# Kernel optimization log

Measured on AMD Instinct MI355X. Metric: run time of the kernel, lower is better.

The kernel has to match this reference:

```python
import jax, jax.numpy as jnp
import numpy as np

N = 50000      # nodes
E = 800000     # edges (avg degree 16)
IN, EMB, HID, OUT = 128, 256, 256, 128
KS = (25000, 12500)  # absolute top-k node counts per pooling level
NEG = -1e9


def setup_inputs() -> dict:
    key = jax.random.key(0)
    k = jax.random.split(key, 20)
    s = 0.05
    rn = lambda kk, shp: (jax.random.normal(kk, shp, jnp.float32) * s)
    return {
        "features": jax.random.normal(k[0], (N, IN), jnp.float32),
        "src": jax.random.randint(k[1], (E,), 0, N, dtype=jnp.int32),
        "dst": jax.random.randint(k[2], (E,), 0, N, dtype=jnp.int32),
        "W_embed": rn(k[3], (IN, EMB)), "b_embed": jnp.zeros((EMB,), jnp.float32),
        "W_enc0": rn(k[4], (EMB, HID)), "b_enc0": jnp.zeros((HID,), jnp.float32),
        "W_enc1": rn(k[5], (HID, HID)), "b_enc1": jnp.zeros((HID,), jnp.float32),
        "W_p0": rn(k[6], (HID, 1)), "b_p0": jnp.zeros((1,), jnp.float32),
        "W_p1": rn(k[7], (HID, 1)), "b_p1": jnp.zeros((1,), jnp.float32),
        "W_bot": rn(k[8], (HID, HID)), "b_bot": jnp.zeros((HID,), jnp.float32),
        "W_dec0": rn(k[9], (HID, HID)), "b_dec0": jnp.zeros((HID,), jnp.float32),
        "W_dec1": rn(k[10], (HID, OUT)), "b_dec1": jnp.zeros((OUT,), jnp.float32),
    }


def _gcn(h, src, dst, emask, W, b, act):
    """DGL GraphConv, norm='both': D_out^{-1/2} A D_in^{-1/2} h W + b, deg clamped >=1.
    emask: float [E] validity mask for edges of the current (sub)graph."""
    n = h.shape[0]
    deg_out = jnp.clip(jax.ops.segment_sum(emask, src, num_segments=n), 1.0)
    deg_in = jnp.clip(jax.ops.segment_sum(emask, dst, num_segments=n), 1.0)
    msg = (h * (deg_out ** -0.5)[:, None])[src] * emask[:, None]  # [E, F]
    agg = jax.ops.segment_sum(msg, dst, num_segments=n)
    out = (agg * (deg_in ** -0.5)[:, None]) @ W + b
    return jax.nn.relu(out) if act else out


def _forward(features, src, dst, W_embed, b_embed, W_enc0, b_enc0, W_enc1, b_enc1,
             W_p0, b_p0, W_p1, b_p1, W_bot, b_bot, W_dec0, b_dec0, W_dec1, b_dec1):
    n = features.shape[0]
    ones_e = jnp.ones((src.shape[0],), features.dtype)
    enc = [(W_enc0, b_enc0), (W_enc1, b_enc1)]
    pools = [(W_p0, b_p0), (W_p1, b_p1)]
    dec = [(W_dec0, b_dec0), (W_dec1, b_dec1)]
    L = len(KS)

    h = _gcn(features, src, dst, ones_e, W_embed, b_embed, True)
    masks = [jnp.ones((n,), features.dtype)]  # node mask per graph level
    hidden = []
    for i in range(L):  # encoder (dropout = eval-mode identity)
        m = masks[i]
        em = m[src] * m[dst]
        h = _gcn(h, src, dst, em, enc[i][0], enc[i][1], True) * m[:, None]
        hidden.append(h)
        # gPool: sigmoid projection score, top-k node selection, gate by score
        scores = jax.nn.sigmoid(h @ pools[i][0] + pools[i][1])[:, 0]
        _, idx = jax.lax.top_k(jnp.where(m > 0, scores, NEG), KS[i])
        nm = jnp.zeros((n,), features.dtype).at[idx].set(1.0)
        h = h * (scores * nm)[:, None]
        masks.append(nm)
    mL = masks[L]
    emL = mL[src] * mL[dst]
    h = _gcn(h, src, dst, emL, W_bot, b_bot, True) * mL[:, None]
    for i in range(L):  # decoder: gUnpool (identity under full-rep masking) + skip + GCN
        j = L - 1 - i
        h = h + hidden[j]
        m = masks[j]
        em = m[src] * m[dst]
        act = i < L - 1  # last decoder layer has no activation
        h = _gcn(h, src, dst, em, dec[i][0], dec[i][1], act) * m[:, None]
    return h


def reference(features, src, dst, W_embed, b_embed, W_enc0, b_enc0, W_enc1, b_enc1,
              W_p0, b_p0, W_p1, b_p1, W_bot, b_bot, W_dec0, b_dec0, W_dec1, b_dec1):
    return _forward(features, src, dst, W_embed, b_embed, W_enc0, b_enc0, W_enc1, b_enc1,
                    W_p0, b_p0, W_p1, b_p1, W_bot, b_bot, W_dec0, b_dec0, W_dec1, b_dec1)
```

## Files before the change

kernel.cpp:

```cpp
#include <hip/hip_runtime.h>
#include <hip/hip_bf16.h>
#include <type_traits>

__global__ void hist_kernel(const int* __restrict__ src, const int* __restrict__ dst,
                            int* __restrict__ deg_out, int* __restrict__ deg_in, int E) {
    int e = blockIdx.x * blockDim.x + threadIdx.x;
    if (e < E) {
        atomicAdd(&deg_out[src[e]], 1);
        atomicAdd(&deg_in[dst[e]], 1);
    }
}

__global__ void scan_kernel(const int* __restrict__ deg, int* __restrict__ row_ptr,
                            int* __restrict__ cursor, int n) {
    __shared__ int wsum[16];
    __shared__ int running;
    int tid = threadIdx.x, lane = tid & 63, wid = tid >> 6;
    if (tid == 0) running = 0;
    __syncthreads();
    for (int base = 0; base < n; base += 1024) {
        int i = base + tid;
        int v = (i < n) ? deg[i] : 0;
        int incl = v;
        #pragma unroll
        for (int off = 1; off < 64; off <<= 1) {
            int t = __shfl_up(incl, off);
            if (lane >= off) incl += t;
        }
        if (lane == 63) wsum[wid] = incl;
        __syncthreads();
        if (wid == 0 && lane < 16) {
            int s = wsum[lane], si = s;
            #pragma unroll
            for (int off = 1; off < 16; off <<= 1) {
                int t = __shfl_up(si, off);
                if (lane >= off) si += t;
            }
            wsum[lane] = si - s;
        }
        __syncthreads();
        int excl = running + wsum[wid] + (incl - v);
        if (i < n) { row_ptr[i] = excl; cursor[i] = excl; }
        __syncthreads();
        if (tid == 1023) running = excl + v;
        __syncthreads();
    }
    if (tid == 0) row_ptr[n] = running;
}

__global__ void fill_kernel(const int* __restrict__ src, const int* __restrict__ dst,
                            int* __restrict__ cursor, int* __restrict__ col, int E) {
    int e = blockIdx.x * blockDim.x + threadIdx.x;
    if (e < E) {
        int p = atomicAdd(&cursor[dst[e]], 1);
        col[p] = src[e];
    }
}

__global__ void sort_rows_kernel(const int* __restrict__ row_ptr, int* __restrict__ col, int n) {
    int v = blockIdx.x * blockDim.x + threadIdx.x;
    if (v >= n) return;
    int e0 = row_ptr[v], e1 = row_ptr[v + 1];
    for (int i = e0 + 1; i < e1; ++i) {
        int key = col[i];
        int j = i - 1;
        while (j >= e0 && col[j] > key) { col[j + 1] = col[j]; --j; }
        col[j + 1] = key;
    }
}

__global__ void out_deg_mask_kernel(const int* __restrict__ src, const int* __restrict__ dst,
                                    const float* __restrict__ m, float* __restrict__ so, int E) {
    int e = blockIdx.x * blockDim.x + threadIdx.x;
    if (e < E) {
        float md = m[dst[e]];
        if (md != 0.f) atomicAdd(&so[src[e]], md);
    }
}

__global__ void in_deg_mask_kernel(const int* __restrict__ row_ptr, const int* __restrict__ col,
                                   const float* __restrict__ m, float* __restrict__ si, int n) {
    int v = blockIdx.x * blockDim.x + threadIdx.x;
    if (v < n) {
        float s = 0.f;
        int e1 = row_ptr[v + 1];
        for (int e = row_ptr[v]; e < e1; ++e) s += m[col[e]];
        si[v] = s;
    }
}

__global__ void scale_full_kernel(const int* __restrict__ dout, const int* __restrict__ din,
                                  float* __restrict__ s, float* __restrict__ t, int n) {
    int v = blockIdx.x * blockDim.x + threadIdx.x;
    if (v < n) {
        s[v] = 1.f / sqrtf((float)max(dout[v], 1));
        t[v] = 1.f / sqrtf((float)max(din[v], 1));
    }
}

__global__ void scale_mask_kernel(const float* __restrict__ gate, const float* __restrict__ mask,
                                  const float* __restrict__ so, const float* __restrict__ si,
                                  float* __restrict__ s, float* __restrict__ t, int n) {
    int v = blockIdx.x * blockDim.x + threadIdx.x;
    if (v < n) {
        s[v] = gate[v] * (1.f / sqrtf(fmaxf(so[v], 1.f)));
        t[v] = mask[v] * (1.f / sqrtf(fmaxf(si[v], 1.f)));
    }
}

__global__ void agg_feat_128_kernel(const int* __restrict__ row_ptr, const int* __restrict__ col,
                                    const float* __restrict__ X, const float* __restrict__ s,
                                    const float* __restrict__ t, float* __restrict__ out, int n) {
    int tid = threadIdx.x;
    int node = blockIdx.x * 8 + (tid >> 5);
    int f4 = tid & 31;
    if (node >= n) return;
    int e0 = row_ptr[node], e1 = row_ptr[node + 1];
    const float4* X4 = (const float4*)X;
    float ax = 0.f, ay = 0.f, az = 0.f, aw = 0.f;
    int e = e0;
    for (; e + 3 < e1; e += 4) {
        int u0 = col[e], u1 = col[e + 1], u2 = col[e + 2], u3 = col[e + 3];
        float s0 = s[u0], s1 = s[u1], s2 = s[u2], s3 = s[u3];
        float4 x0 = X4[(size_t)u0 * 32 + f4];
        float4 x1 = X4[(size_t)u1 * 32 + f4];
        float4 x2 = X4[(size_t)u2 * 32 + f4];
        float4 x3 = X4[(size_t)u3 * 32 + f4];
        ax += s0 * x0.x; ay += s0 * x0.y; az += s0 * x0.z; aw += s0 * x0.w;
        ax += s1 * x1.x; ay += s1 * x1.y; az += s1 * x1.z; aw += s1 * x1.w;
        ax += s2 * x2.x; ay += s2 * x2.y; az += s2 * x2.z; aw += s2 * x2.w;
        ax += s3 * x3.x; ay += s3 * x3.y; az += s3 * x3.z; aw += s3 * x3.w;
    }
    for (; e < e1; ++e) {
        int u = col[e];
        float sc = s[u];
        float4 q = X4[(size_t)u * 32 + f4];
        ax += sc * q.x; ay += sc * q.y; az += sc * q.z; aw += sc * q.w;
    }
    float tv = t[node];
    float4 r; r.x = ax * tv; r.y = ay * tv; r.z = az * tv; r.w = aw * tv;
    ((float4*)out)[(size_t)node * 32 + f4] = r;
}

template <bool MASKED>
__global__ void agg_f32_256_kernel(const int* __restrict__ row_ptr, const int* __restrict__ col,
                                   const float* __restrict__ X, const float* __restrict__ s,
                                   const float* __restrict__ t, float* __restrict__ out, int n) {
    int tid = threadIdx.x;
    int node = blockIdx.x * 4 + (tid >> 6);
    int f4 = tid & 63;
    if (node >= n) return;
    float tv = t[node];
    if (MASKED && tv == 0.f) return;
    int e0 = row_ptr[node], e1 = row_ptr[node + 1];
    const float4* X4 = (const float4*)X;
    float ax = 0.f, ay = 0.f, az = 0.f, aw = 0.f;
    int e = e0;
    for (; e + 3 < e1; e += 4) {
        int u0 = col[e], u1 = col[e + 1], u2 = col[e + 2], u3 = col[e + 3];
        float s0 = s[u0], s1 = s[u1], s2 = s[u2], s3 = s[u3];
        if (!MASKED) {
            float4 x0 = X4[(size_t)u0 * 64 + f4];
            float4 x1 = X4[(size_t)u1 * 64 + f4];
            float4 x2 = X4[(size_t)u2 * 64 + f4];
            float4 x3 = X4[(size_t)u3 * 64 + f4];
            ax += s0 * x0.x; ay += s0 * x0.y; az += s0 * x0.z; aw += s0 * x0.w;
            ax += s1 * x1.x; ay += s1 * x1.y; az += s1 * x1.z; aw += s1 * x1.w;
            ax += s2 * x2.x; ay += s2 * x2.y; az += s2 * x2.z; aw += s2 * x2.w;
            ax += s3 * x3.x; ay += s3 * x3.y; az += s3 * x3.z; aw += s3 * x3.w;
        } else {
            if (s0 != 0.f) { float4 x = X4[(size_t)u0 * 64 + f4];
                ax += s0 * x.x; ay += s0 * x.y; az += s0 * x.z; aw += s0 * x.w; }
            if (s1 != 0.f) { float4 x = X4[(size_t)u1 * 64 + f4];
                ax += s1 * x.x; ay += s1 * x.y; az += s1 * x.z; aw += s1 * x.w; }
            if (s2 != 0.f) { float4 x = X4[(size_t)u2 * 64 + f4];
                ax += s2 * x.x; ay += s2 * x.y; az += s2 * x.z; aw += s2 * x.w; }
            if (s3 != 0.f) { float4 x = X4[(size_t)u3 * 64 + f4];
                ax += s3 * x.x; ay += s3 * x.y; az += s3 * x.z; aw += s3 * x.w; }
        }
    }
    for (; e < e1; ++e) {
        int u = col[e];
        float sc = s[u];
        if (!MASKED || sc != 0.f) {
            float4 xv = X4[(size_t)u * 64 + f4];
            ax += sc * xv.x; ay += sc * xv.y; az += sc * xv.z; aw += sc * xv.w;
        }
    }
    float4 r; r.x = ax * tv; r.y = ay * tv; r.z = az * tv; r.w = aw * tv;
    ((float4*)out)[(size_t)node * 64 + f4] = r;
}

__global__ void agg_bias_128_kernel(const int* __restrict__ row_ptr, const int* __restrict__ col,
                                    const float* __restrict__ P, const float* __restrict__ t,
                                    const float* __restrict__ bias, float* __restrict__ out, int n) {
    int tid = threadIdx.x;
    int node = blockIdx.x * 8 + (tid >> 5);
    int f4 = tid & 31;
    if (node >= n) return;
    int e0 = row_ptr[node], e1 = row_ptr[node + 1];
    const float4* P4 = (const float4*)P;
    float ax = 0.f, ay = 0.f, az = 0.f, aw = 0.f;
    int e = e0;
    for (; e + 3 < e1; e += 4) {
        int u0 = col[e], u1 = col[e + 1], u2 = col[e + 2], u3 = col[e + 3];
        float4 x0 = P4[(size_t)u0 * 32 + f4];
        float4 x1 = P4[(size_t)u1 * 32 + f4];
        float4 x2 = P4[(size_t)u2 * 32 + f4];
        float4 x3 = P4[(size_t)u3 * 32 + f4];
        ax += x0.x; ay += x0.y; az += x0.z; aw += x0.w;
        ax += x1.x; ay += x1.y; az += x1.z; aw += x1.w;
        ax += x2.x; ay += x2.y; az += x2.z; aw += x2.w;
        ax += x3.x; ay += x3.y; az += x3.z; aw += x3.w;
    }
    for (; e < e1; ++e) {
        int u = col[e];
        float4 q = P4[(size_t)u * 32 + f4];
        ax += q.x; ay += q.y; az += q.z; aw += q.w;
    }
    float tv = t[node];
    float4 bv = ((const float4*)bias)[f4];
    float4 r;
    r.x = ax * tv + bv.x; r.y = ay * tv + bv.y;
    r.z = az * tv + bv.z; r.w = aw * tv + bv.w;
    ((float4*)out)[(size_t)node * 32 + f4] = r;
}

template <bool RELU>
__global__ __launch_bounds__(256) void gemm_kernel(const float* __restrict__ A,
                                                   const float* __restrict__ W,
                                                   const float* __restrict__ bias,
                                                   const float* __restrict__ mask,
                                                   const float* __restrict__ rowscale,
                                                   float* __restrict__ C, int M, int K, int Nn) {
    __shared__ float As[16][68];
    __shared__ float Bs[16][132];
    int tid = threadIdx.x;
    int bm = blockIdx.x * 64, bn = blockIdx.y * 128;
    int mA = tid >> 2, kqA = (tid & 3) * 4;
    int kB = tid >> 4, nqB = (tid & 15) * 8;
    int tm = (tid >> 4) * 4, tn = (tid & 15) * 4;
    float acc[4][8] = {};
    float rs = rowscale ? rowscale[bm + mA] : 1.f;
    for (int k0 = 0; k0 < K; k0 += 16) {
        float4 av = *(const float4*)(A + (size_t)(bm + mA) * K + k0 + kqA);
        As[kqA + 0][mA] = av.x * rs; As[kqA + 1][mA] = av.y * rs;
        As[kqA + 2][mA] = av.z * rs; As[kqA + 3][mA] = av.w * rs;
        const float* wp = W + (size_t)(k0 + kB) * Nn + bn + nqB;
        *(float4*)&Bs[kB][nqB]     = *(const float4*)wp;
        *(float4*)&Bs[kB][nqB + 4] = *(const float4*)(wp + 4);
        __syncthreads();
        #pragma unroll
        for (int kk = 0; kk < 16; ++kk) {
            float4 a  = *(const float4*)&As[kk][tm];
            float4 b0 = *(const float4*)&Bs[kk][tn];
            float4 b1 = *(const float4*)&Bs[kk][tn + 64];
            float ar[4] = {a.x, a.y, a.z, a.w};
            float br[8] = {b0.x, b0.y, b0.z, b0.w, b1.x, b1.y, b1.z, b1.w};
            #pragma unroll
            for (int i2 = 0; i2 < 4; i2++)
                #pragma unroll
                for (int j = 0; j < 8; j++) acc[i2][j] += ar[i2] * br[j];
        }
        __syncthreads();
    }
    #pragma unroll
    for (int i2 = 0; i2 < 4; i2++) {
        int row = bm + tm + i2;
        if (row < M) {
            float mv = mask ? mask[row] : 1.f;
            float o[8];
            #pragma unroll
            for (int j = 0; j < 8; j++) {
                int cj = (j < 4) ? (tn + j) : (64 + tn + j - 4);
                float x = acc[i2][j] + (bias ? bias[bn + cj] : 0.f);
                if (RELU) x = fmaxf(x, 0.f);
                o[j] = x * mv;
            }
            float* cp = C + (size_t)row * Nn + bn;
            *(float4*)(cp + tn)      = make_float4(o[0], o[1], o[2], o[3]);
            *(float4*)(cp + 64 + tn) = make_float4(o[4], o[5], o[6], o[7]);
        }
    }
}

template <bool RELU>
__global__ __launch_bounds__(256) void gemm_rows_kernel(const float* __restrict__ A,
                                                        const float* __restrict__ W,
                                                        const float* __restrict__ bias,
                                                        const int* __restrict__ idx, int Mc,
                                                        float* __restrict__ C, int K, int Nn) {
    __shared__ float As[16][68];
    __shared__ float Bs[16][132];
    __shared__ int ridx[64];
    int tid = threadIdx.x;
    int bm = blockIdx.x * 64, bn = blockIdx.y * 128;
    if (tid < 64) {
        int r = bm + tid;
        ridx[tid] = (r < Mc) ? idx[r] : idx[0];
    }
    __syncthreads();
    int mA = tid >> 2, kqA = (tid & 3) * 4;
    int kB = tid >> 4, nqB = (tid & 15) * 8;
    int tm = (tid >> 4) * 4, tn = (tid & 15) * 4;
    int rA = ridx[mA];
    float acc[4][8] = {};
    for (int k0 = 0; k0 < K; k0 += 16) {
        float4 av = *(const float4*)(A + (size_t)rA * K + k0 + kqA);
        As[kqA + 0][mA] = av.x; As[kqA + 1][mA] = av.y;
        As[kqA + 2][mA] = av.z; As[kqA + 3][mA] = av.w;
        const float* wp = W + (size_t)(k0 + kB) * Nn + bn + nqB;
        *(float4*)&Bs[kB][nqB]     = *(const float4*)wp;
        *(float4*)&Bs[kB][nqB + 4] = *(const float4*)(wp + 4);
        __syncthreads();
        #pragma unroll
        for (int kk = 0; kk < 16; ++kk) {
            float4 a  = *(const float4*)&As[kk][tm];
            float4 b0 = *(const float4*)&Bs[kk][tn];
            float4 b1 = *(const float4*)&Bs[kk][tn + 64];
            float ar[4] = {a.x, a.y, a.z, a.w};
            float br[8] = {b0.x, b0.y, b0.z, b0.w, b1.x, b1.y, b1.z, b1.w};
            #pragma unroll
            for (int i2 = 0; i2 < 4; i2++)
                #pragma unroll
                for (int j = 0; j < 8; j++) acc[i2][j] += ar[i2] * br[j];
        }
        __syncthreads();
    }
    #pragma unroll
    for (int i2 = 0; i2 < 4; i2++) {
        int r = bm + tm + i2;
        if (r < Mc) {
            int row = ridx[tm + i2];
            float o[8];
            #pragma unroll
            for (int j = 0; j < 8; j++) {
                int cj = (j < 4) ? (tn + j) : (64 + tn + j - 4);
                float x = acc[i2][j] + bias[bn + cj];
                if (RELU) x = fmaxf(x, 0.f);
                o[j] = x;
            }
            float* cp = C + (size_t)row * Nn + bn;
            *(float4*)(cp + tn)      = make_float4(o[0], o[1], o[2], o[3]);
            *(float4*)(cp + 64 + tn) = make_float4(o[4], o[5], o[6], o[7]);
        }
    }
}

__global__ void score_kernel(const float* __restrict__ H, const float* __restrict__ Wp,
                             const float* __restrict__ bp, const float* __restrict__ mask,
                             float* __restrict__ scores, float* __restrict__ keys, int n) {
    int lane = threadIdx.x & 63;
    int node = blockIdx.x * 4 + (threadIdx.x >> 6);
    if (node >= n) return;
    float4 hv = ((const float4*)(H + (size_t)node * 256))[lane];
    float4 wq = ((const float4*)Wp)[lane];
    float d = hv.x * wq.x + hv.y * wq.y + hv.z * wq.z + hv.w * wq.w;
    #pragma unroll
    for (int off = 32; off > 0; off >>= 1) d += __shfl_down(d, off);
    if (lane == 0) {
        float sc = 1.f / (1.f + expf(-(d + bp[0])));
        scores[node] = sc;
        keys[node] = (mask && mask[node] == 0.f) ? -1e9f : sc;
    }
}

__device__ __forceinline__ unsigned key_u(float f) {
    unsigned u = __float_as_uint(f);
    return (u & 0x80000000u) ? ~u : (u | 0x80000000u);
}

__device__ __forceinline__ void wave_hist_add(int* __restrict__ hist, unsigned bin, bool valid) {
    int lane = threadIdx.x & 63;
    while (true) {
        unsigned long long vmask = __ballot(valid);
        if (vmask == 0ull) break;
        int leader = __ffsll((long long)vmask) - 1;
        unsigned lbin = (unsigned)__shfl((int)bin, leader);
        bool match = valid && (bin == lbin);
        unsigned long long mmask = __ballot(match);
        if (lane == leader) atomicAdd(&hist[lbin], __popcll(mmask));
        if (match) valid = false;
    }
}

__global__ void topk_kernel(const float* __restrict__ keys, const float* __restrict__ scores,
                            float* __restrict__ nm, float* __restrict__ gate, int n, int K) {
    __shared__ int hist[256];
    __shared__ unsigned sh_prefix;
    __shared__ int sh_krem;
    __shared__ int sh_running;
    __shared__ int wsum[16];
    int tid = threadIdx.x, lane = tid & 63, wid = tid >> 6;
    if (tid == 0) { sh_prefix = 0u; sh_krem = K; sh_running = 0; }
    __syncthreads();
    for (int pass = 0; pass < 4; ++pass) {
        int shift = 24 - pass * 8;
        if (tid < 256) hist[tid] = 0;
        __syncthreads();
        unsigned pmask = (pass == 0) ? 0u : (0xFFFFFFFFu << (shift + 8));
        unsigned prefix = sh_prefix;
        for (int i = tid; i < n; i += 1024) {
            unsigned u = key_u(keys[i]);
            if ((u & pmask) == prefix) atomicAdd(&hist[(u >> shift) & 0xFF], 1);
        }
        __syncthreads();
        if (tid == 0) {
            int krem = sh_krem;
            int b;
            for (b = 255; b > 0; --b) {
                int c = hist[b];
                if (c >= krem) break;
                krem -= c;
            }
            sh_prefix = prefix | ((unsigned)b << shift);
            sh_krem = krem;
        }
        __syncthreads();
    }
    unsigned Tkey = sh_prefix;
    int need_eq = sh_krem;
    for (int base = 0; base < n; base += 1024) {
        int i = base + tid;
        unsigned u = 0; int flagv = 0;
        if (i < n) { u = key_u(keys[i]); flagv = (u == Tkey) ? 1 : 0; }
        unsigned long long bal = __ballot(flagv);
        int rank_w = __popcll(bal & ((1ull << lane) - 1ull));
        if (lane == 63) wsum[wid] = __popcll(bal);
        __syncthreads();
        int woff = 0;
        for (int w = 0; w < wid; ++w) woff += wsum[w];
        int grank = sh_running + woff + rank_w;
        if (i < n) {
            float v = (u > Tkey) ? 1.f : ((flagv && grank < need_eq) ? 1.f : 0.f);
            nm[i] = v;
            gate[i] = v * scores[i];
        }
        __syncthreads();
        if (tid == 0) {
            int tot = 0;
            for (int w = 0; w < 16; ++w) tot += wsum[w];
            sh_running += tot;
        }
        __syncthreads();
    }
}

__global__ void topk_hist1(const float* __restrict__ keys, int n, int* __restrict__ hist) {
    int i = blockIdx.x * blockDim.x + threadIdx.x;
    unsigned bin = 0; bool valid = (i < n);
    if (valid) bin = key_u(keys[i]) >> 16;
    wave_hist_add(hist, bin, valid);
}

__global__ void topk_scan1(const int* __restrict__ hist, int K, int* __restrict__ sel) {
    __shared__ int arr[1024];
    int tid = threadIdx.x;
    int base = tid * 64;
    int local = 0;
    #pragma unroll 8
    for (int b = 0; b < 64; ++b) local += hist[base + b];
    arr[tid] = local;
    __syncthreads();
    for (int off = 1; off < 1024; off <<= 1) {
        int v = (tid + off < 1024) ? arr[tid + off] : 0;
        __syncthreads();
        arr[tid] += v;
        __syncthreads();
    }
    int above = arr[tid] - local;
    if (above < K && arr[tid] >= K) {
        int run = above;
        for (int b = base + 63; b >= base; --b) {
            int c = hist[b];
            if (run + c >= K) { sel[0] = b; sel[1] = K - run; break; }
            run += c;
        }
    }
}

__global__ void topk_hist2(const float* __restrict__ keys, int n, const int* __restrict__ sel,
                           int* __restrict__ hist) {
    int i = blockIdx.x * blockDim.x + threadIdx.x;
    unsigned bin = 0; bool valid = false;
    if (i < n) {
        unsigned u = key_u(keys[i]);
        if ((int)(u >> 16) == sel[0]) { bin = u & 0xFFFF; valid = true; }
    }
    wave_hist_add(hist, bin, valid);
}

__global__ void topk_scan2(const int* __restrict__ hist, int* __restrict__ sel,
                           int* __restrict__ tie_cnt) {
    __shared__ int arr[1024];
    int tid = threadIdx.x;
    if (tid == 0) *tie_cnt = 0;
    int K = sel[1];
    int base = tid * 64;
    int local = 0;
    #pragma unroll 8
    for (int b = 0; b < 64; ++b) local += hist[base + b];
    arr[tid] = local;
    __syncthreads();
    for (int off = 1; off < 1024; off <<= 1) {
        int v = (tid + off < 1024) ? arr[tid + off] : 0;
        __syncthreads();
        arr[tid] += v;
        __syncthreads();
    }
    int above = arr[tid] - local;
    if (above < K && arr[tid] >= K) {
        int run = above;
        for (int b = base + 63; b >= base; --b) {
            int c = hist[b];
            if (run + c >= K) {
                sel[2] = (int)((((unsigned)sel[0]) << 16) | (unsigned)b);
                sel[3] = K - run;
                break;
            }
            run += c;
        }
    }
}

__global__ void topk_mark(const float* __restrict__ keys, const float* __restrict__ scores,
                          const int* __restrict__ sel, float* __restrict__ nm,
                          float* __restrict__ gate, int* __restrict__ tie_list,
                          int* __restrict__ tie_cnt, int n) {
    int i = blockIdx.x * blockDim.x + threadIdx.x;
    if (i >= n) return;
    unsigned Tkey = (unsigned)sel[2];
    unsigned u = key_u(keys[i]);
    float v = 0.f;
    if (u > Tkey) v = 1.f;
    else if (u == Tkey) { int p = atomicAdd(tie_cnt, 1); tie_list[p] = i; }
    nm[i] = v;
    gate[i] = v * scores[i];
}

__global__ void topk_ties(const float* __restrict__ scores, const int* __restrict__ sel,
                          const int* __restrict__ tie_list, const int* __restrict__ tie_cnt,
                          float* __restrict__ nm, float* __restrict__ gate) {
    int cnt = *tie_cnt;
    int need = sel[3];
    for (int j = threadIdx.x; j < cnt; j += blockDim.x) {
        int idx = tie_list[j];
        int rank = 0;
        for (int k2 = 0; k2 < cnt; ++k2) rank += (tie_list[k2] < idx) ? 1 : 0;
        if (rank < need) { nm[idx] = 1.f; gate[idx] = scores[idx]; }
    }
}

__global__ void compact_kernel(const float* __restrict__ nm, int* __restrict__ idx,
                               int* __restrict__ cnt, int n) {
    int i = blockIdx.x * blockDim.x + threadIdx.x;
    if (i < n && nm[i] != 0.f) {
        int p = atomicAdd(cnt, 1);
        idx[p] = i;
    }
}

__global__ void add_mask_kernel(float* __restrict__ A, const float* __restrict__ B,
                                const float* __restrict__ mask, int n4) {
    int i = blockIdx.x * blockDim.x + threadIdx.x;
    if (i < n4) {
        float4 a = ((float4*)A)[i];
        float4 b = ((const float4*)B)[i];
        if (mask && mask[i >> 6] == 0.f) { a.x = 0.f; a.y = 0.f; a.z = 0.f; a.w = 0.f; }
        a.x += b.x; a.y += b.y; a.z += b.z; a.w += b.w;
        ((float4*)A)[i] = a;
    }
}

extern "C" void kernel_launch(void* const* d_in, const int* in_sizes, int n_in,
                              void* d_out, int out_size, void* d_ws, size_t ws_size,
                              hipStream_t stream) {
    const int n = in_sizes[0] / 128;
    const int E = in_sizes[1];
    const int NPAD = ((n + 63) / 64) * 64;
    const int K1 = 25000, K2 = 12500;

    const float* features = (const float*)d_in[0];
    const int* src = (const int*)d_in[1];
    const int* dst = (const int*)d_in[2];
    const float* W_embed = (const float*)d_in[3];
    const float* b_embed = (const float*)d_in[4];
    const float* W_enc0  = (const float*)d_in[5];
    const float* b_enc0  = (const float*)d_in[6];
    const float* W_enc1  = (const float*)d_in[7];
    const float* b_enc1  = (const float*)d_in[8];
    const float* W_p0    = (const float*)d_in[9];
    const float* b_p0    = (const float*)d_in[10];
    const float* W_p1    = (const float*)d_in[11];
    const float* b_p1    = (const float*)d_in[12];
    const float* W_bot   = (const float*)d_in[13];
    const float* b_bot   = (const float*)d_in[14];
    const float* W_dec0  = (const float*)d_in[15];
    const float* b_dec0  = (const float*)d_in[16];
    const float* W_dec1  = (const float*)d_in[17];
    const float* b_dec1  = (const float*)d_in[18];
    float* out_f = (float*)d_out;

    char* ws = (char*)d_ws;
    size_t off = 0;
    auto alloc = [&](size_t bytes) -> void* {
        void* p = ws + off;
        off += (bytes + 255) & ~(size_t)255;
        return p;
    };
    (void)alloc(256);
    int* row_ptr  = (int*)alloc((size_t)(n + 1) * 4);
    int* cursor   = (int*)alloc((size_t)n * 4);
    int* col      = (int*)alloc((size_t)E * 4);
    int* deg_out_i= (int*)alloc((size_t)n * 4);
    int* deg_in_i = (int*)alloc((size_t)n * 4);
    float* so_m1  = (float*)alloc((size_t)n * 4);
    float* si_m1  = (float*)alloc((size_t)n * 4);
    float* so_m2  = (float*)alloc((size_t)n * 4);
    float* si_m2  = (float*)alloc((size_t)n * 4);
    float* sarr   = (float*)alloc((size_t)n * 4);
    float* tarr   = (float*)alloc((size_t)n * 4);
    float* scores1= (float*)alloc((size_t)n * 4);
    float* keys1  = (float*)alloc((size_t)n * 4);
    float* scores2= (float*)alloc((size_t)n * 4);
    float* keys2  = (float*)alloc((size_t)n * 4);
    float* nm1    = (float*)alloc((size_t)n * 4);
    float* gate1  = (float*)alloc((size_t)n * 4);
    float* nm2    = (float*)alloc((size_t)n * 4);
    float* gate2  = (float*)alloc((size_t)n * 4);
    size_t big = (size_t)NPAD * 256 * 4;
    float* A = (float*)alloc(big);
    float* B = (float*)alloc(big);
    float* C = (float*)alloc(big);
    float* D = (float*)alloc(big);
    int* rhist    = (int*)alloc(65536 * 4);
    int* sel      = (int*)alloc(256);
    int* tie_cnt  = (int*)alloc(256);
    int* tie_list = (int*)alloc((size_t)n * 4);
    float* s0     = (float*)alloc((size_t)n * 4);
    float* t0     = (float*)alloc((size_t)n * 4);
    int* idx1     = (int*)alloc((size_t)n * 4);
    int* idx2     = (int*)alloc((size_t)n * 4);
    int* ccnt     = (int*)alloc(256);
    bool fast = (off <= ws_size);

    dim3 blk(256);
    int gE = (E + 255) / 256;
    int gN = (n + 255) / 256;
    int gAgg256 = (n + 3) / 4;
    int gAgg128 = (n + 7) / 8;
    int gScore = (n + 3) / 4;
    dim3 gemm_g(NPAD / 64, 2);
    dim3 gemm_g128(NPAD / 64, 1);
    dim3 gemm_gK1((K1 + 63) / 64, 2);
    dim3 gemm_gK2((K2 + 63) / 64, 2);
    int gAdd = (n * 64 + 255) / 256;

    auto run_topk = [&](const float* keys, const float* scores, float* nm, float* gate, int K) {
        if (fast) {
            hipMemsetAsync(rhist, 0, 65536 * 4, stream);
            topk_hist1<<<gN, blk, 0, stream>>>(keys, n, rhist);
            topk_scan1<<<1, 1024, 0, stream>>>(rhist, K, sel);
            hipMemsetAsync(rhist, 0, 65536 * 4, stream);
            topk_hist2<<<gN, blk, 0, stream>>>(keys, n, sel, rhist);
            topk_scan2<<<1, 1024, 0, stream>>>(rhist, sel, tie_cnt);
            topk_mark<<<gN, blk, 0, stream>>>(keys, scores, sel, nm, gate, tie_list, tie_cnt, n);
            topk_ties<<<1, 256, 0, stream>>>(scores, sel, tie_list, tie_cnt, nm, gate);
        } else {
            topk_kernel<<<1, 1024, 0, stream>>>(keys, scores, nm, gate, n, K);
        }
    };
    float* sF = fast ? s0 : sarr;
    float* tF = fast ? t0 : tarr;

    hipMemsetAsync(deg_out_i, 0, (size_t)n * 4, stream);
    hipMemsetAsync(deg_in_i, 0, (size_t)n * 4, stream);
    hist_kernel<<<gE, blk, 0, stream>>>(src, dst, deg_out_i, deg_in_i, E);
    scan_kernel<<<1, 1024, 0, stream>>>(deg_in_i, row_ptr, cursor, n);
    fill_kernel<<<gE, blk, 0, stream>>>(src, dst, cursor, col, E);
    sort_rows_kernel<<<gN, blk, 0, stream>>>(row_ptr, col, n);

    scale_full_kernel<<<gN, blk, 0, stream>>>(deg_out_i, deg_in_i, sF, tF, n);

    agg_feat_128_kernel<<<gAgg128, blk, 0, stream>>>(row_ptr, col, features, sF, tF, D, n);
    gemm_kernel<true><<<gemm_g, blk, 0, stream>>>(D, W_embed, b_embed, nullptr, nullptr, A, n, 128, 256);

    agg_f32_256_kernel<false><<<gAgg256, blk, 0, stream>>>(row_ptr, col, A, sF, tF, D, n);
    gemm_kernel<true><<<gemm_g, blk, 0, stream>>>(D, W_enc0, b_enc0, nullptr, nullptr, B, n, 256, 256);

    score_kernel<<<gScore, blk, 0, stream>>>(B, W_p0, b_p0, nullptr, scores1, keys1, n);
    run_topk(keys1, scores1, nm1, gate1, K1);
    if (fast) {
        hipMemsetAsync(ccnt, 0, 4, stream);
        compact_kernel<<<gN, blk, 0, stream>>>(nm1, idx1, ccnt, n);
    }

    hipMemsetAsync(so_m1, 0, (size_t)n * 4, stream);
    out_deg_mask_kernel<<<gE, blk, 0, stream>>>(src, dst, nm1, so_m1, E);
    in_deg_mask_kernel<<<gN, blk, 0, stream>>>(row_ptr, col, nm1, si_m1, n);
    scale_mask_kernel<<<gN, blk, 0, stream>>>(gate1, nm1, so_m1, si_m1, sarr, tarr, n);
    agg_f32_256_kernel<true><<<gAgg256, blk, 0, stream>>>(row_ptr, col, B, sarr, tarr, D, n);
    if (fast)
        gemm_rows_kernel<true><<<gemm_gK1, blk, 0, stream>>>(D, W_enc1, b_enc1, idx1, K1, C, 256, 256);
    else
        gemm_kernel<true><<<gemm_g, blk, 0, stream>>>(D, W_enc1, b_enc1, nm1, nullptr, C, n, 256, 256);

    score_kernel<<<gScore, blk, 0, stream>>>(C, W_p1, b_p1, nm1, scores2, keys2, n);
    run_topk(keys2, scores2, nm2, gate2, K2);
    if (fast) {
        hipMemsetAsync(ccnt + 1, 0, 4, stream);
        compact_kernel<<<gN, blk, 0, stream>>>(nm2, idx2, ccnt + 1, n);
    }

    hipMemsetAsync(so_m2, 0, (size_t)n * 4, stream);
    out_deg_mask_kernel<<<gE, blk, 0, stream>>>(src, dst, nm2, so_m2, E);
    in_deg_mask_kernel<<<gN, blk, 0, stream>>>(row_ptr, col, nm2, si_m2, n);
    scale_mask_kernel<<<gN, blk, 0, stream>>>(gate2, nm2, so_m2, si_m2, sarr, tarr, n);
    agg_f32_256_kernel<true><<<gAgg256, blk, 0, stream>>>(row_ptr, col, C, sarr, tarr, D, n);
    if (fast)
        gemm_rows_kernel<true><<<gemm_gK2, blk, 0, stream>>>(D, W_bot, b_bot, idx2, K2, A, 256, 256);
    else
        gemm_kernel<true><<<gemm_g, blk, 0, stream>>>(D, W_bot, b_bot, nm2, nullptr, A, n, 256, 256);

    add_mask_kernel<<<gAdd, blk, 0, stream>>>(A, C, fast ? nm2 : nullptr, n * 64);
    scale_mask_kernel<<<gN, blk, 0, stream>>>(nm1, nm1, so_m1, si_m1, sarr, tarr, n);
    agg_f32_256_kernel<true><<<gAgg256, blk, 0, stream>>>(row_ptr, col, A, sarr, tarr, D, n);
    if (fast)
        gemm_rows_kernel<true><<<gemm_gK1, blk, 0, stream>>>(D, W_dec0, b_dec0, idx1, K1, A, 256, 256);
    else
        gemm_kernel<true><<<gemm_g, blk, 0, stream>>>(D, W_dec0, b_dec0, nm1, nullptr, A, n, 256, 256);

    add_mask_kernel<<<gAdd, blk, 0, stream>>>(A, B, fast ? nm1 : nullptr, n * 64);
    if (!fast)
        scale_full_kernel<<<gN, blk, 0, stream>>>(deg_out_i, deg_in_i, sarr, tarr, n);
    gemm_kernel<false><<<gemm_g128, blk, 0, stream>>>(A, W_dec1, nullptr, nullptr, sF, C, n, 256, 128);
    agg_bias_128_kernel<<<gAgg128, blk, 0, stream>>>(row_ptr, col, C, tF, b_dec1, out_f, n);

    (void)n_in; (void)out_size;
}
```

Measured before the change: 1.346 ms.

## Replace FP32 SIMT GEMMs with split-bf16 MFMA GEMMs

Adds a kernel that splits each weight matrix once per call into transposed bf16 high and low parts. All dense GEMMs, full and row-gathered, move to MFMA kernels that split activations on the fly and run three bf16 MFMAs (hi*hi, hi*lo, lo*hi) to approximate FP32 accuracy. This aims to replace the scalar FMA inner loops with matrix-core throughput, at the cost of extra conversion work, doubled shared-memory traffic and some precision loss. The old row-gathered FP32 GEMM is removed and the FP32 GEMM is kept as the fallback.

```diff
diff --git a/kernel.cpp b/kernel.cpp
--- a/kernel.cpp
+++ b/kernel.cpp
@@ -226,6 +226,225 @@
     ((float4*)out)[(size_t)node * 32 + f4] = r;
 }
 
+
+__device__ __forceinline__ unsigned short f2bf(float x) {
+    unsigned u = __float_as_uint(x);
+    unsigned r = u + 0x7fffu + ((u >> 16) & 1u);
+    return (unsigned short)(r >> 16);
+}
+__device__ __forceinline__ float bf2f(unsigned short h) {
+    return __uint_as_float(((unsigned)h) << 16);
+}
+
+typedef __attribute__((ext_vector_type(8))) short short8v;
+typedef __attribute__((ext_vector_type(4))) float f32x4;
+
+__global__ void wsplit_all_kernel(const float* __restrict__ W0, const float* __restrict__ W1,
+                                  const float* __restrict__ W2, const float* __restrict__ W3,
+                                  const float* __restrict__ W4, const float* __restrict__ W5,
+                                  unsigned short* __restrict__ H, unsigned short* __restrict__ L) {
+    int i = blockIdx.x * blockDim.x + threadIdx.x;
+    const float* W; int rel, base, outIdx;
+    if (i < 32768) { W = W0; rel = i; base = 0;
+        int k = rel >> 8, nn = rel & 255; outIdx = nn * 128 + k; }
+    else if (i < 98304) { W = W1; rel = i - 32768; base = 32768;
+        int k = rel >> 8, nn = rel & 255; outIdx = nn * 256 + k; }
+    else if (i < 163840) { W = W2; rel = i - 98304; base = 98304;
+        int k = rel >> 8, nn = rel & 255; outIdx = nn * 256 + k; }
+    else if (i < 229376) { W = W3; rel = i - 163840; base = 163840;
+        int k = rel >> 8, nn = rel & 255; outIdx = nn * 256 + k; }
+    else if (i < 294912) { W = W4; rel = i - 229376; base = 229376;
+        int k = rel >> 8, nn = rel & 255; outIdx = nn * 256 + k; }
+    else { W = W5; rel = i - 294912; base = 294912;
+        int k = rel >> 7, nn = rel & 127; outIdx = nn * 256 + k; }
+    float x = W[rel];
+    unsigned short h = f2bf(x);
+    H[base + outIdx] = h;
+    L[base + outIdx] = f2bf(x - bf2f(h));
+}
+
+template <bool RELU>
+__global__ __launch_bounds__(256) void gemm_mfma_kernel(
+    const float* __restrict__ A, const unsigned short* __restrict__ Wh,
+    const unsigned short* __restrict__ Wl, const float* __restrict__ bias,
+    const float* __restrict__ rowscale, float* __restrict__ C, int M, int K, int Nn) {
+    __shared__ __align__(16) short sAh[64][40];
+    __shared__ __align__(16) short sAl[64][40];
+    __shared__ __align__(16) short sWh[128][40];
+    __shared__ __align__(16) short sWl[128][40];
+    int tid = threadIdx.x;
+    int bm = blockIdx.x * 64, bn = blockIdx.y * 128;
+    int lane = tid & 63, wid = tid >> 6;
+    int lr = lane & 15, kg = lane >> 4;
+    int arow = tid >> 2, akq = (tid & 3) * 8;
+    int wn = tid >> 1, wkh = (tid & 1) * 16;
+    float rs = rowscale ? rowscale[bm + arow] : 1.f;
+    const float* aptr = A + (size_t)(bm + arow) * K + akq;
+    const unsigned short* whp = Wh + (size_t)(bn + wn) * K + wkh;
+    const unsigned short* wlp = Wl + (size_t)(bn + wn) * K + wkh;
+    f32x4 acc[4][2];
+    #pragma unroll
+    for (int i = 0; i < 4; ++i)
+        #pragma unroll
+        for (int j = 0; j < 2; ++j) acc[i][j] = (f32x4){0.f, 0.f, 0.f, 0.f};
+    for (int k0 = 0; k0 < K; k0 += 32) {
+        float4 a0 = *(const float4*)(aptr + k0);
+        float4 a1 = *(const float4*)(aptr + k0 + 4);
+        float f[8] = {a0.x * rs, a0.y * rs, a0.z * rs, a0.w * rs,
+                      a1.x * rs, a1.y * rs, a1.z * rs, a1.w * rs};
+        short8v Hv, Lv;
+        #pragma unroll
+        for (int j = 0; j < 8; ++j) {
+            unsigned short h = f2bf(f[j]);
+            Hv[j] = (short)h;
+            Lv[j] = (short)f2bf(f[j] - bf2f(h));
+        }
+        short8v w0 = *(const short8v*)(whp + k0);
+        short8v w1 = *(const short8v*)(whp + k0 + 8);
+        short8v w2 = *(const short8v*)(wlp + k0);
+        short8v w3 = *(const short8v*)(wlp + k0 + 8);
+        __syncthreads();
+        *(short8v*)&sAh[arow][akq] = Hv;
+        *(short8v*)&sAl[arow][akq] = Lv;
+        *(short8v*)&sWh[wn][wkh] = w0;
+        *(short8v*)&sWh[wn][wkh + 8] = w1;
+        *(short8v*)&sWl[wn][wkh] = w2;
+        *(short8v*)&sWl[wn][wkh + 8] = w3;
+        __syncthreads();
+        short8v ah[4], al[4], bh[2], bl[2];
+        #pragma unroll
+        for (int mf = 0; mf < 4; ++mf) {
+            ah[mf] = *(const short8v*)&sAh[mf * 16 + lr][kg * 8];
+            al[mf] = *(const short8v*)&sAl[mf * 16 + lr][kg * 8];
+        }
+        #pragma unroll
+        for (int nf = 0; nf < 2; ++nf) {
+            int c = wid * 32 + nf * 16 + lr;
+            bh[nf] = *(const short8v*)&sWh[c][kg * 8];
+            bl[nf] = *(const short8v*)&sWl[c][kg * 8];
+        }
+        #pragma unroll
+        for (int mf = 0; mf < 4; ++mf)
+            #pragma unroll
+            for (int nf = 0; nf < 2; ++nf) {
+                acc[mf][nf] = __builtin_amdgcn_mfma_f32_16x16x32_bf16(ah[mf], bh[nf], acc[mf][nf], 0, 0, 0);
+                acc[mf][nf] = __builtin_amdgcn_mfma_f32_16x16x32_bf16(ah[mf], bl[nf], acc[mf][nf], 0, 0, 0);
+                acc[mf][nf] = __builtin_amdgcn_mfma_f32_16x16x32_bf16(al[mf], bh[nf], acc[mf][nf], 0, 0, 0);
+            }
+    }
+    #pragma unroll
+    for (int mf = 0; mf < 4; ++mf) {
+        #pragma unroll
+        for (int nf = 0; nf < 2; ++nf) {
+            int col = bn + wid * 32 + nf * 16 + lr;
+            float bv = bias ? bias[col] : 0.f;
+            #pragma unroll
+            for (int r = 0; r < 4; ++r) {
+                int grow = bm + mf * 16 + kg * 4 + r;
+                if (grow < M) {
+                    float x = acc[mf][nf][r] + bv;
+                    if (RELU) x = fmaxf(x, 0.f);
+                    C[(size_t)grow * Nn + col] = x;
+                }
+            }
+        }
+    }
+}
+
+template <bool RELU>
+__global__ __launch_bounds__(256) void gemm_rows_mfma_kernel(
+    const float* __restrict__ A, const unsigned short* __restrict__ Wh,
+    const unsigned short* __restrict__ Wl, const float* __restrict__ bias,
+    const int* __restrict__ idx, int Mc, float* __restrict__ C, int K, int Nn) {
+    __shared__ __align__(16) short sAh[64][40];
+    __shared__ __align__(16) short sAl[64][40];
+    __shared__ __align__(16) short sWh[128][40];
+    __shared__ __align__(16) short sWl[128][40];
+    __shared__ int ridx[64];
+    int tid = threadIdx.x;
+    int bm = blockIdx.x * 64, bn = blockIdx.y * 128;
+    int lane = tid & 63, wid = tid >> 6;
+    int lr = lane & 15, kg = lane >> 4;
+    int arow = tid >> 2, akq = (tid & 3) * 8;
+    int wn = tid >> 1, wkh = (tid & 1) * 16;
+    if (tid < 64) {
+        int r = bm + tid;
+        ridx[tid] = (r < Mc) ? idx[r] : idx[0];
+    }
+    __syncthreads();
+    int rA = ridx[arow];
+    const float* aptr = A + (size_t)rA * K + akq;
+    const unsigned short* whp = Wh + (size_t)(bn + wn) * K + wkh;
+    const unsigned short* wlp = Wl + (size_t)(bn + wn) * K + wkh;
+    f32x4 acc[4][2];
+    #pragma unroll
+    for (int i = 0; i < 4; ++i)
+        #pragma unroll
+        for (int j = 0; j < 2; ++j) acc[i][j] = (f32x4){0.f, 0.f, 0.f, 0.f};
+    for (int k0 = 0; k0 < K; k0 += 32) {
+        float4 a0 = *(const float4*)(aptr + k0);
+        float4 a1 = *(const float4*)(aptr + k0 + 4);
+        float f[8] = {a0.x, a0.y, a0.z, a0.w, a1.x, a1.y, a1.z, a1.w};
+        short8v Hv, Lv;
+        #pragma unroll
+        for (int j = 0; j < 8; ++j) {
+            unsigned short h = f2bf(f[j]);
+            Hv[j] = (short)h;
+            Lv[j] = (short)f2bf(f[j] - bf2f(h));
+        }
+        short8v w0 = *(const short8v*)(whp + k0);
+        short8v w1 = *(const short8v*)(whp + k0 + 8);
+        short8v w2 = *(const short8v*)(wlp + k0);
+        short8v w3 = *(const short8v*)(wlp + k0 + 8);
+        __syncthreads();
+        *(short8v*)&sAh[arow][akq] = Hv;
+        *(short8v*)&sAl[arow][akq] = Lv;
+        *(short8v*)&sWh[wn][wkh] = w0;
+        *(short8v*)&sWh[wn][wkh + 8] = w1;
+        *(short8v*)&sWl[wn][wkh] = w2;
+        *(short8v*)&sWl[wn][wkh + 8] = w3;
+        __syncthreads();
+        short8v ah[4], al[4], bh[2], bl[2];
+        #pragma unroll
+        for (int mf = 0; mf < 4; ++mf) {
+            ah[mf] = *(const short8v*)&sAh[mf * 16 + lr][kg * 8];
+            al[mf] = *(const short8v*)&sAl[mf * 16 + lr][kg * 8];
+        }
+        #pragma unroll
+        for (int nf = 0; nf < 2; ++nf) {
+            int c = wid * 32 + nf * 16 + lr;
+            bh[nf] = *(const short8v*)&sWh[c][kg * 8];
+            bl[nf] = *(const short8v*)&sWl[c][kg * 8];
+        }
+        #pragma unroll
+        for (int mf = 0; mf < 4; ++mf)
+            #pragma unroll
+            for (int nf = 0; nf < 2; ++nf) {
+                acc[mf][nf] = __builtin_amdgcn_mfma_f32_16x16x32_bf16(ah[mf], bh[nf], acc[mf][nf], 0, 0, 0);
+                acc[mf][nf] = __builtin_amdgcn_mfma_f32_16x16x32_bf16(ah[mf], bl[nf], acc[mf][nf], 0, 0, 0);
+                acc[mf][nf] = __builtin_amdgcn_mfma_f32_16x16x32_bf16(al[mf], bh[nf], acc[mf][nf], 0, 0, 0);
+            }
+    }
+    #pragma unroll
+    for (int mf = 0; mf < 4; ++mf) {
+        #pragma unroll
+        for (int nf = 0; nf < 2; ++nf) {
+            int col = bn + wid * 32 + nf * 16 + lr;
+            float bv = bias[col];
+            #pragma unroll
+            for (int r = 0; r < 4; ++r) {
+                int lrow = mf * 16 + kg * 4 + r;
+                if (bm + lrow < Mc) {
+                    int grow = ridx[lrow];
+                    float x = acc[mf][nf][r] + bv;
+                    if (RELU) x = fmaxf(x, 0.f);
+                    C[(size_t)grow * Nn + col] = x;
+                }
+            }
+        }
+    }
+}
+
 template <bool RELU>
 __global__ __launch_bounds__(256) void gemm_kernel(const float* __restrict__ A,
                                                    const float* __restrict__ W,
@@ -276,69 +495,6 @@
                 float x = acc[i2][j] + (bias ? bias[bn + cj] : 0.f);
                 if (RELU) x = fmaxf(x, 0.f);
                 o[j] = x * mv;
-            }
-            float* cp = C + (size_t)row * Nn + bn;
-            *(float4*)(cp + tn)      = make_float4(o[0], o[1], o[2], o[3]);
-            *(float4*)(cp + 64 + tn) = make_float4(o[4], o[5], o[6], o[7]);
-        }
-    }
-}
-
-template <bool RELU>
-__global__ __launch_bounds__(256) void gemm_rows_kernel(const float* __restrict__ A,
-                                                        const float* __restrict__ W,
-                                                        const float* __restrict__ bias,
-                                                        const int* __restrict__ idx, int Mc,
-                                                        float* __restrict__ C, int K, int Nn) {
-    __shared__ float As[16][68];
-    __shared__ float Bs[16][132];
-    __shared__ int ridx[64];
-    int tid = threadIdx.x;
-    int bm = blockIdx.x * 64, bn = blockIdx.y * 128;
-    if (tid < 64) {
-        int r = bm + tid;
-        ridx[tid] = (r < Mc) ? idx[r] : idx[0];
-    }
-    __syncthreads();
-    int mA = tid >> 2, kqA = (tid & 3) * 4;
-    int kB = tid >> 4, nqB = (tid & 15) * 8;
-    int tm = (tid >> 4) * 4, tn = (tid & 15) * 4;
-    int rA = ridx[mA];
-    float acc[4][8] = {};
-    for (int k0 = 0; k0 < K; k0 += 16) {
-        float4 av = *(const float4*)(A + (size_t)rA * K + k0 + kqA);
-        As[kqA + 0][mA] = av.x; As[kqA + 1][mA] = av.y;
-        As[kqA + 2][mA] = av.z; As[kqA + 3][mA] = av.w;
-        const float* wp = W + (size_t)(k0 + kB) * Nn + bn + nqB;
-        *(float4*)&Bs[kB][nqB]     = *(const float4*)wp;
-        *(float4*)&Bs[kB][nqB + 4] = *(const float4*)(wp + 4);
-        __syncthreads();
-        #pragma unroll
-        for (int kk = 0; kk < 16; ++kk) {
-            float4 a  = *(const float4*)&As[kk][tm];
-            float4 b0 = *(const float4*)&Bs[kk][tn];
-            float4 b1 = *(const float4*)&Bs[kk][tn + 64];
-            float ar[4] = {a.x, a.y, a.z, a.w};
-            float br[8] = {b0.x, b0.y, b0.z, b0.w, b1.x, b1.y, b1.z, b1.w};
-            #pragma unroll
-            for (int i2 = 0; i2 < 4; i2++)
-                #pragma unroll
-                for (int j = 0; j < 8; j++) acc[i2][j] += ar[i2] * br[j];
-        }
-        __syncthreads();
-    }
-    #pragma unroll
-    for (int i2 = 0; i2 < 4; i2++) {
-        int r = bm + tm + i2;
-        if (r < Mc) {
-            int row = ridx[tm + i2];
-            float o[8];
-            #pragma unroll
-            for (int j = 0; j < 8; j++) {
-                int cj = (j < 4) ? (tn + j) : (64 + tn + j - 4);
-                float x = acc[i2][j] + bias[bn + cj];
-                if (RELU) x = fmaxf(x, 0.f);
-                o[j] = x;
             }
             float* cp = C + (size_t)row * Nn + bn;
             *(float4*)(cp + tn)      = make_float4(o[0], o[1], o[2], o[3]);
@@ -642,6 +798,11 @@
     int* idx1     = (int*)alloc((size_t)n * 4);
     int* idx2     = (int*)alloc((size_t)n * 4);
     int* ccnt     = (int*)alloc(256);
+    const int WO_EMBED = 0, WO_ENC0 = 32768, WO_ENC1 = 98304,
+              WO_BOT = 163840, WO_DEC0 = 229376, WO_DEC1 = 294912;
+    const int WTOT = 327680;
+    unsigned short* wsph = (unsigned short*)alloc((size_t)WTOT * 2);
+    unsigned short* wspl = (unsigned short*)alloc((size_t)WTOT * 2);
     bool fast = (off <= ws_size);
 
     dim3 blk(256);
@@ -673,6 +834,11 @@
     float* sF = fast ? s0 : sarr;
     float* tF = fast ? t0 : tarr;
 
+    if (fast) {
+        wsplit_all_kernel<<<WTOT / 256, blk, 0, stream>>>(W_embed, W_enc0, W_enc1, W_bot,
+                                                          W_dec0, W_dec1, wsph, wspl);
+    }
+
     hipMemsetAsync(deg_out_i, 0, (size_t)n * 4, stream);
     hipMemsetAsync(deg_in_i, 0, (size_t)n * 4, stream);
     hist_kernel<<<gE, blk, 0, stream>>>(src, dst, deg_out_i, deg_in_i, E);
@@ -683,10 +849,18 @@
     scale_full_kernel<<<gN, blk, 0, stream>>>(deg_out_i, deg_in_i, sF, tF, n);
 
     agg_feat_128_kernel<<<gAgg128, blk, 0, stream>>>(row_ptr, col, features, sF, tF, D, n);
-    gemm_kernel<true><<<gemm_g, blk, 0, stream>>>(D, W_embed, b_embed, nullptr, nullptr, A, n, 128, 256);
+    if (fast)
+        gemm_mfma_kernel<true><<<gemm_g, blk, 0, stream>>>(D, wsph + WO_EMBED, wspl + WO_EMBED,
+                                                           b_embed, nullptr, A, n, 128, 256);
+    else
+        gemm_kernel<true><<<gemm_g, blk, 0, stream>>>(D, W_embed, b_embed, nullptr, nullptr, A, n, 128, 256);
 
     agg_f32_256_kernel<false><<<gAgg256, blk, 0, stream>>>(row_ptr, col, A, sF, tF, D, n);
-    gemm_kernel<true><<<gemm_g, blk, 0, stream>>>(D, W_enc0, b_enc0, nullptr, nullptr, B, n, 256, 256);
+    if (fast)
+        gemm_mfma_kernel<true><<<gemm_g, blk, 0, stream>>>(D, wsph + WO_ENC0, wspl + WO_ENC0,
+                                                           b_enc0, nullptr, B, n, 256, 256);
+    else
+        gemm_kernel<true><<<gemm_g, blk, 0, stream>>>(D, W_enc0, b_enc0, nullptr, nullptr, B, n, 256, 256);
 
     score_kernel<<<gScore, blk, 0, stream>>>(B, W_p0, b_p0, nullptr, scores1, keys1, n);
     run_topk(keys1, scores1, nm1, gate1, K1);
@@ -701,7 +875,8 @@
     scale_mask_kernel<<<gN, blk, 0, stream>>>(gate1, nm1, so_m1, si_m1, sarr, tarr, n);
     agg_f32_256_kernel<true><<<gAgg256, blk, 0, stream>>>(row_ptr, col, B, sarr, tarr, D, n);
     if (fast)
-        gemm_rows_kernel<true><<<gemm_gK1, blk, 0, stream>>>(D, W_enc1, b_enc1, idx1, K1, C, 256, 256);
+        gemm_rows_mfma_kernel<true><<<gemm_gK1, blk, 0, stream>>>(D, wsph + WO_ENC1, wspl + WO_ENC1,
+                                                                  b_enc1, idx1, K1, C, 256, 256);
     else
         gemm_kernel<true><<<gemm_g, blk, 0, stream>>>(D, W_enc1, b_enc1, nm1, nullptr, C, n, 256, 256);
 
@@ -718,7 +893,8 @@
     scale_mask_kernel<<<gN, blk, 0, stream>>>(gate2, nm2, so_m2, si_m2, sarr, tarr, n);
     agg_f32_256_kernel<true><<<gAgg256, blk, 0, stream>>>(row_ptr, col, C, sarr, tarr, D, n);
     if (fast)
-        gemm_rows_kernel<true><<<gemm_gK2, blk, 0, stream>>>(D, W_bot, b_bot, idx2, K2, A, 256, 256);
+        gemm_rows_mfma_kernel<true><<<gemm_gK2, blk, 0, stream>>>(D, wsph + WO_BOT, wspl + WO_BOT,
+                                                                  b_bot, idx2, K2, A, 256, 256);
     else
         gemm_kernel<true><<<gemm_g, blk, 0, stream>>>(D, W_bot, b_bot, nm2, nullptr, A, n, 256, 256);
 
@@ -726,14 +902,19 @@
     scale_mask_kernel<<<gN, blk, 0, stream>>>(nm1, nm1, so_m1, si_m1, sarr, tarr, n);
     agg_f32_256_kernel<true><<<gAgg256, blk, 0, stream>>>(row_ptr, col, A, sarr, tarr, D, n);
     if (fast)
-        gemm_rows_kernel<true><<<gemm_gK1, blk, 0, stream>>>(D, W_dec0, b_dec0, idx1, K1, A, 256, 256);
+        gemm_rows_mfma_kernel<true><<<gemm_gK1, blk, 0, stream>>>(D, wsph + WO_DEC0, wspl + WO_DEC0,
+                                                                  b_dec0, idx1, K1, A, 256, 256);
     else
         gemm_kernel<true><<<gemm_g, blk, 0, stream>>>(D, W_dec0, b_dec0, nm1, nullptr, A, n, 256, 256);
 
     add_mask_kernel<<<gAdd, blk, 0, stream>>>(A, B, fast ? nm1 : nullptr, n * 64);
     if (!fast)
         scale_full_kernel<<<gN, blk, 0, stream>>>(deg_out_i, deg_in_i, sarr, tarr, n);
-    gemm_kernel<false><<<gemm_g128, blk, 0, stream>>>(A, W_dec1, nullptr, nullptr, sF, C, n, 256, 128);
+    if (fast)
+        gemm_mfma_kernel<false><<<gemm_g128, blk, 0, stream>>>(A, wsph + WO_DEC1, wspl + WO_DEC1,
+                                                               nullptr, sF, C, n, 256, 128);
+    else
+        gemm_kernel<false><<<gemm_g128, blk, 0, stream>>>(A, W_dec1, nullptr, nullptr, sF, C, n, 256, 128);
     agg_bias_128_kernel<<<gAgg128, blk, 0, stream>>>(row_ptr, col, C, tF, b_dec1, out_f, n);
 
     (void)n_in; (void)out_size;
```

New measurement: 1.149 ms. -14.7%, faster.
